# Performance work log

Hardware: AMD Instinct MI355X
Metric: run time of the kernel (lower is better)

Reference implementation:

```python
import jax, jax.numpy as jnp
import numpy as np

B, S, D = 2, 2048, 2048
H, KV = 16, 4          # n_heads, n_kv_heads
HD = D // H            # head_dim = 128
FFN = 5632
EPS = 1e-6


def rmsnorm(t, w):
    return (t * jax.lax.rsqrt(jnp.mean(t * t, axis=-1, keepdims=True) + EPS)) * w


def setup_inputs() -> dict:
    key = jax.random.key(0)
    ks = jax.random.split(key, 12)
    # rotary tables: cos/sin stacked in last dim -> [S, HD//2, 2]
    inv_freq = 1.0 / (10000.0 ** (np.arange(0, HD, 2, dtype=np.float32) / HD))
    t = np.arange(S, dtype=np.float32)
    ang = np.einsum('s,f->sf', t, inv_freq)
    freqs_cis = jnp.asarray(np.stack([np.cos(ang), np.sin(ang)], axis=-1))
    p = lambda k, shape: jax.random.normal(k, shape, dtype=jnp.float32) * 0.02
    return {
        'x': jax.random.normal(ks[0], (B, S, D), dtype=jnp.float32),
        'velocity': jnp.zeros((B, S, D), dtype=jnp.float32),
        'freqs_cis': freqs_cis,
        'pre_norm_w': jnp.ones((D,), jnp.float32),
        'wq': p(ks[1], (D, H * HD)),
        'wk': p(ks[2], (D, KV * HD)),
        'wv': p(ks[3], (D, KV * HD)),
        'wo': p(ks[4], (H * HD, D)),
        'q_norm_w': jnp.ones((HD,), jnp.float32),
        'k_norm_w': jnp.ones((HD,), jnp.float32),
        'log_beta': jnp.float32(np.log(0.5 / 0.5)),  # sigmoid -> 0.5
        'ffn_norm_w': jnp.ones((D,), jnp.float32),
        'w1': p(ks[5], (D, FFN)),
        'w3': p(ks[6], (D, FFN)),
        'w2': p(ks[7], (FFN, D)),
    }


def _rope(t, cos, sin):
    # t: [B,S,h,HD]; cos/sin broadcast [1,S,1,HD//2]
    tr = t.reshape(*t.shape[:-1], HD // 2, 2)
    t0, t1 = tr[..., 0], tr[..., 1]
    return jnp.stack([t0 * cos - t1 * sin, t0 * sin + t1 * cos], axis=-1).reshape(t.shape)


def reference(x, velocity, freqs_cis, pre_norm_w, wq, wk, wv, wo,
              q_norm_w, k_norm_w, log_beta, ffn_norm_w, w1, w3, w2):
    h = rmsnorm(x, pre_norm_w)
    q = (h @ wq).reshape(B, S, H, HD)
    k = (h @ wk).reshape(B, S, KV, HD)
    v = (h @ wv).reshape(B, S, KV, HD)
    # qk-norm (per-head RMSNorm), then rotary
    q = rmsnorm(q, q_norm_w)
    k = rmsnorm(k, k_norm_w)
    cos = freqs_cis[None, :, None, :, 0]
    sin = freqs_cis[None, :, None, :, 1]
    q = _rope(q, cos, sin)
    k = _rope(k, cos, sin)
    # GQA: repeat kv heads
    k = jnp.repeat(k, H // KV, axis=2)
    v = jnp.repeat(v, H // KV, axis=2)
    scores = jnp.einsum('bqhd,bkhd->bhqk', q, k) / jnp.float32(np.sqrt(HD))
    # exclusive self-attention: attend strictly to past (j < i); row 0 -> zeros
    excl = jnp.tril(jnp.ones((S, S), bool), k=-1)
    probs = jax.nn.softmax(jnp.where(excl, scores, jnp.float32(-1e30)), axis=-1)
    probs = probs * excl  # exact zeros on masked cols; row 0 fully zero
    attn_out = jnp.einsum('bhqk,bkhd->bqhd', probs, v).reshape(B, S, D) @ wo
    # sigmoid-gated momentum residual with clamp
    beta = jax.nn.sigmoid(log_beta)
    velocity = jnp.clip(beta * velocity + attn_out, -8.0, 8.0)
    x = x + velocity
    # inlined RMSNorm recompute + SwiGLU FFN
    normed = rmsnorm(x, ffn_norm_w)
    ffn = (jax.nn.silu(normed @ w1) * (normed @ w3)) @ w2
    return (x + ffn, velocity)
```

## Files before the change

kernel.cpp:

```cpp
#include <hip/hip_runtime.h>
#include <cstdint>
#include <cstddef>

typedef __bf16 bf16;
typedef __bf16 bf16x2 __attribute__((ext_vector_type(2)));
typedef __bf16 bf16x8 __attribute__((ext_vector_type(8)));
typedef float  f32x4  __attribute__((ext_vector_type(4)));

#define DEV __device__ __forceinline__

constexpr int Bc = 2, Sc = 2048, Dc = 2048, Hc = 16, KVc = 4, HDc = 128, FFNc = 5632;
constexpr int Rc = Bc * Sc;

DEV void async16(const bf16* g, bf16* l) {
  __builtin_amdgcn_global_load_lds((const __attribute__((address_space(1))) void*)g,
                                   (__attribute__((address_space(3))) void*)l, 16, 0, 0);
}

__global__ void transpose_cast(const float* __restrict__ in, bf16* __restrict__ out,
                               int K, int N, int rowoff, int ldout) {
  __shared__ float tile[32][33];
  int k0 = blockIdx.y * 32, n0 = blockIdx.x * 32;
  int tx = threadIdx.x, ty = threadIdx.y;
  for (int r = ty; r < 32; r += 8)
    tile[r][tx] = in[(size_t)(k0 + r) * N + n0 + tx];
  __syncthreads();
  for (int r = ty; r < 32; r += 8)
    out[(size_t)(rowoff + n0 + r) * ldout + k0 + tx] = (bf16)tile[tx][r];
}

__global__ void transpose_v(const bf16* __restrict__ qkvb, bf16* __restrict__ vht) {
  __shared__ bf16 tile[32][33];
  int s0 = blockIdx.x * 32, d0 = blockIdx.y * 32, bg = blockIdx.z;
  int tx = threadIdx.x, ty = threadIdx.y;
  int b = bg >> 2, g = bg & 3;
  const bf16* src = qkvb + (size_t)(b * Sc) * 3072 + 2560 + g * 128;
  for (int r = ty; r < 32; r += 8)
    tile[r][tx] = src[(size_t)(s0 + r) * 3072 + d0 + tx];
  __syncthreads();
  bf16* dst = vht + ((size_t)bg * HDc) * Sc;
  for (int r = ty; r < 32; r += 8)
    dst[(size_t)(d0 + r) * Sc + s0 + tx] = tile[tx][r];
}

__global__ void rmsnorm_cast(const float* __restrict__ x, const float* __restrict__ w,
                             bf16* __restrict__ out) {
  __shared__ float red[4];
  int row = blockIdx.x, tid = threadIdx.x;
  const float* xr = x + (size_t)row * Dc;
  float ss = 0.f;
#pragma unroll
  for (int i = 0; i < Dc / 256; ++i) { float v = xr[tid + i * 256]; ss += v * v; }
  for (int off = 32; off; off >>= 1) ss += __shfl_xor(ss, off);
  if ((tid & 63) == 0) red[tid >> 6] = ss;
  __syncthreads();
  float rstd = rsqrtf((red[0] + red[1] + red[2] + red[3]) * (1.f / Dc) + 1e-6f);
  bf16* orow = out + (size_t)row * Dc;
#pragma unroll
  for (int i = 0; i < Dc / 256; ++i) {
    int j = tid + i * 256;
    orow[j] = (bf16)(xr[j] * rstd * w[j]);
  }
}

DEV int swzofs(int r, int quad) {
  int pr = r >> 1;
  int g = (((r & 1) << 2) | quad) ^ (pr & 7);
  return pr * 64 + g * 8;
}

template <int MODE, int NF>
__global__ __launch_bounds__(512, 2) void gemm256(
    const bf16* __restrict__ A, int lda, const bf16* __restrict__ Bt,
    float* __restrict__ Cf, bf16* __restrict__ Cb,
    const float* __restrict__ xin, const float* __restrict__ velin,
    const float* __restrict__ lbp, float* __restrict__ velout,
    int K, int ldc, int nbx) {
  constexpr int BN = NF * 64;
  constexpr int BLD = 2 + BN / 128;
  __shared__ bf16 Asb[3][256 * 32];
  __shared__ bf16 Bsb[3][BN * 32];
  const int tid = threadIdx.x, lane = tid & 63, w = tid >> 6;
  const int quad = lane >> 4, l15 = lane & 15;
  const int wm = w >> 2, wn = w & 3;

  const int nwg = gridDim.x, bid = blockIdx.x;
  const int qq = nwg >> 3, rr = nwg & 7, xcd = bid & 7, lid = bid >> 3;
  const int swz = (xcd < rr ? xcd * (qq + 1) : rr * (qq + 1) + (xcd - rr) * qq) + lid;
  const int m0 = (swz / nbx) * 256, n0 = (swz % nbx) * BN;

  const int NT = K >> 5;

  f32x4 acc[8][NF];
  const f32x4 zf = {0.f, 0.f, 0.f, 0.f};
#pragma unroll
  for (int i = 0; i < 8; ++i)
#pragma unroll
    for (int j = 0; j < NF; ++j) acc[i][j] = zf;

  auto stage = [&](int kt, int ring) {
    const int k0 = kt * 32;
#pragma unroll
    for (int i = 0; i < 2; ++i) {
      int fi = w * 2 + i;
      int pr = fi * 8 + (lane >> 3), g0 = (lane & 7) ^ (pr & 7);
      int r = pr * 2 + (g0 >> 2), c8 = (g0 & 3) * 8;
      async16(A + (size_t)(m0 + r) * lda + k0 + c8, Asb[ring] + fi * 512);
    }
#pragma unroll
    for (int i = 0; i < BN / 128; ++i) {
      int fi = w * (BN / 128) + i;
      int pr = fi * 8 + (lane >> 3), g0 = (lane & 7) ^ (pr & 7);
      int r = pr * 2 + (g0 >> 2), c8 = (g0 & 3) * 8;
      async16(Bt + (size_t)(n0 + r) * K + k0 + c8, Bsb[ring] + fi * 512);
    }
  };

  stage(0, 0);
  stage(1, 1);
  if constexpr (BLD == 4) asm volatile("s_waitcnt vmcnt(4)" ::: "memory");
  else                    asm volatile("s_waitcnt vmcnt(3)" ::: "memory");
  __builtin_amdgcn_s_barrier();

  int r0 = 0;
  for (int kt = 0; kt < NT; ++kt) {
    int r2 = r0 + 2; if (r2 >= 3) r2 -= 3;
    const bf16* Ak = Asb[r0];
    const bf16* Bk = Bsb[r0];
    if (kt + 2 < NT) stage(kt + 2, r2);

    bf16x8 bfr[NF], af[4];
#pragma unroll
    for (int j = 0; j < NF; ++j)
      bfr[j] = *(const bf16x8*)(Bk + swzofs(wn * (NF * 16) + j * 16 + l15, quad));
#pragma unroll
    for (int i = 0; i < 4; ++i)
      af[i] = *(const bf16x8*)(Ak + swzofs(wm * 128 + i * 16 + l15, quad));
    __builtin_amdgcn_s_barrier();
    __builtin_amdgcn_s_setprio(1);
#pragma unroll
    for (int i = 0; i < 4; ++i)
#pragma unroll
      for (int j = 0; j < NF; ++j)
        acc[i][j] = __builtin_amdgcn_mfma_f32_16x16x32_bf16(af[i], bfr[j], acc[i][j], 0, 0, 0);
    __builtin_amdgcn_s_setprio(0);
    __builtin_amdgcn_s_barrier();

#pragma unroll
    for (int i = 0; i < 4; ++i)
      af[i] = *(const bf16x8*)(Ak + swzofs(wm * 128 + 64 + i * 16 + l15, quad));
    __builtin_amdgcn_s_barrier();
    __builtin_amdgcn_s_setprio(1);
#pragma unroll
    for (int i = 0; i < 4; ++i)
#pragma unroll
      for (int j = 0; j < NF; ++j)
        acc[4 + i][j] = __builtin_amdgcn_mfma_f32_16x16x32_bf16(af[i], bfr[j], acc[4 + i][j], 0, 0, 0);
    __builtin_amdgcn_s_setprio(0);

    if (kt + 2 < NT) {
      if constexpr (BLD == 4) asm volatile("s_waitcnt vmcnt(4)" ::: "memory");
      else                    asm volatile("s_waitcnt vmcnt(3)" ::: "memory");
    } else if (kt + 2 == NT) {
      asm volatile("s_waitcnt vmcnt(0)" ::: "memory");
    }
    __builtin_amdgcn_sched_barrier(0);
    __builtin_amdgcn_s_barrier();
    r0 = (r0 == 2) ? 0 : r0 + 1;
  }

  float beta = 0.f;
  if (MODE == 1) beta = 1.f / (1.f + __expf(-lbp[0]));
#pragma unroll
  for (int i = 0; i < 8; ++i) {
#pragma unroll
    for (int j = 0; j < NF; ++j) {
#pragma unroll
      for (int r = 0; r < 4; ++r) {
        int row = m0 + wm * 128 + i * 16 + quad * 4 + r;
        int col = n0 + wn * (NF * 16) + j * 16 + l15;
        size_t idx = (size_t)row * ldc + col;
        float c = acc[i][j][r];
        if (MODE == 1) {
          float v = beta * velin[idx] + c;
          v = fminf(8.f, fmaxf(-8.f, v));
          velout[idx] = v;
          Cf[idx] = xin[idx] + v;
        } else if (MODE == 2) {
          Cb[idx] = (bf16)c;
        } else {
          Cf[idx] = xin[idx] + c;
        }
      }
    }
  }
}

__global__ __launch_bounds__(256) void qk_norm_rope(
    const bf16* __restrict__ qkv, const float* __restrict__ qw, const float* __restrict__ kw,
    const float* __restrict__ freqs, bf16* __restrict__ qh, bf16* __restrict__ kh) {
  int row = blockIdx.x;
  int b = row >> 11, s = row & 2047;
  int tid = threadIdx.x, wvid = tid >> 6, lane = tid & 63;
  float cs = freqs[(size_t)(s * 64 + lane) * 2 + 0];
  float sn = freqs[(size_t)(s * 64 + lane) * 2 + 1];
  for (int slot = wvid; slot < 20; slot += 4) {
    const bf16* base = qkv + (size_t)row * 3072 + slot * 128;
    float t0 = (float)base[2 * lane], t1 = (float)base[2 * lane + 1];
    float ss = t0 * t0 + t1 * t1;
    for (int off = 32; off; off >>= 1) ss += __shfl_xor(ss, off);
    float rstd = rsqrtf(ss * (1.f / 128.f) + 1e-6f);
    const float* w = (slot < 16) ? qw : kw;
    float sc = (slot < 16) ? 0.08838834764831845f : 1.f;
    float n0 = t0 * rstd * w[2 * lane], n1 = t1 * rstd * w[2 * lane + 1];
    bf16x2 o;
    o[0] = (bf16)((n0 * cs - n1 * sn) * sc);
    o[1] = (bf16)((n0 * sn + n1 * cs) * sc);
    if (slot < 16)
      *(bf16x2*)(qh + ((size_t)(b * Hc + slot) * Sc + s) * HDc + 2 * lane) = o;
    else
      *(bf16x2*)(kh + ((size_t)(b * KVc + (slot - 16)) * Sc + s) * HDc + 2 * lane) = o;
  }
}

__global__ __launch_bounds__(256) void flash_attn(
    const bf16* __restrict__ qh, const bf16* __restrict__ kh, const bf16* __restrict__ vht,
    bf16* __restrict__ attn) {
  __shared__ bf16 Ks[2][64 * 128];
  __shared__ bf16 Vs[2][128 * 64];
  __shared__ bf16 Ps[4][16 * 68];
  const int tid = threadIdx.x, lane = tid & 63, wvid = tid >> 6;
  const int quad = lane >> 4, l15 = lane & 15;
  const int pairp = blockIdx.x;
  const int h = blockIdx.y, b = blockIdx.z, g = h >> 2;
  const bf16* qbase = qh + (size_t)(b * Hc + h) * Sc * HDc;
  const bf16* kbase = kh + (size_t)(b * KVc + g) * Sc * HDc;
  const bf16* vbase = vht + (size_t)(b * KVc + g) * HDc * Sc;
  const f32x4 zf = {0.f, 0.f, 0.f, 0.f};
  bf16* pw = Ps[wvid];

  bf16x8 ones;
#pragma unroll
  for (int e = 0; e < 8; ++e) ones[e] = (bf16)1.0f;

  int kcol[4], vcol[2];
#pragma unroll
  for (int f = 0; f < 4; ++f) kcol[f] = ((f * 64 + quad * 16) ^ (l15 << 4)) >> 1;
#pragma unroll
  for (int ks = 0; ks < 2; ++ks) vcol[ks] = ((ks * 64 + quad * 16) ^ ((l15 & 7) << 4)) >> 1;

  auto stage = [&](int kt2, int bsel) {
    const int k0s = kt2 * 64;
#pragma unroll
    for (int r = 0; r < 4; ++r) {
      int krow = (wvid * 4 + r) * 4 + quad;
      const bf16* src = kbase + (size_t)(k0s + krow) * HDc + ((l15 ^ (krow & 15)) * 8);
      async16(src, &Ks[bsel][(wvid * 4 + r) * 512]);
    }
#pragma unroll
    for (int r = 0; r < 4; ++r) {
      int vrow = (wvid * 4 + r) * 8 + (lane >> 3);
      int c8 = lane & 7;
      const bf16* src = vbase + (size_t)vrow * Sc + k0s + ((c8 ^ (vrow & 7)) * 8);
      async16(src, &Vs[bsel][(wvid * 4 + r) * 512]);
    }
  };

  for (int pass = 0; pass < 2; ++pass) {
    const int qt = pass ? 31 - pairp : pairp;
    const int q0 = qt * 64 + wvid * 16;

    bf16x8 qf[4];
#pragma unroll
    for (int f = 0; f < 4; ++f)
      qf[f] = *(const bf16x8*)(qbase + (size_t)(q0 + l15) * HDc + f * 32 + quad * 8);

    f32x4 Oa[8];
#pragma unroll
    for (int i = 0; i < 8; ++i) Oa[i] = zf;
    float m_i[4], l_i[4];
#pragma unroll
    for (int r = 0; r < 4; ++r) { m_i[r] = -3e38f; l_i[r] = 0.f; }

    const int ntiles = qt + 1;

    __syncthreads();
    stage(0, 0);

    for (int kt = 0; kt < ntiles; ++kt) {
      const int buf = kt & 1;
      const int k0 = kt * 64;
      __syncthreads();
      if (kt + 1 < ntiles) stage(kt + 1, buf ^ 1);

      f32x4 sc[4];
#pragma unroll
      for (int ks = 0; ks < 4; ++ks) {
        sc[ks] = zf;
#pragma unroll
        for (int f = 0; f < 4; ++f) {
          bf16x8 kf = *(const bf16x8*)(&Ks[buf][ks * 2048 + l15 * 128 + kcol[f]]);
          sc[ks] = __builtin_amdgcn_mfma_f32_16x16x32_bf16(qf[f], kf, sc[ks], 0, 0, 0);
        }
      }

      if (kt == qt) {
#pragma unroll
        for (int r = 0; r < 4; ++r) {
          int qg = q0 + quad * 4 + r;
#pragma unroll
          for (int ks = 0; ks < 4; ++ks)
            if (k0 + ks * 16 + l15 >= qg) sc[ks][r] = -3e38f;
        }
      }

      float mx[4], al[4];
#pragma unroll
      for (int r = 0; r < 4; ++r)
        mx[r] = fmaxf(fmaxf(sc[0][r], sc[1][r]), fmaxf(sc[2][r], sc[3][r]));
#pragma unroll
      for (int off = 8; off; off >>= 1)
#pragma unroll
        for (int r = 0; r < 4; ++r) mx[r] = fmaxf(mx[r], __shfl_xor(mx[r], off));
#pragma unroll
      for (int r = 0; r < 4; ++r) {
        float mn = fmaxf(m_i[r], mx[r]);
        al[r] = __expf(m_i[r] - mn);
        m_i[r] = mn;
#pragma unroll
        for (int ks = 0; ks < 4; ++ks) {
          float p = (sc[ks][r] > -1e37f) ? __expf(sc[ks][r] - mn) : 0.f;
          sc[ks][r] = p;
        }
      }

#pragma unroll
      for (int r = 0; r < 4; ++r)
#pragma unroll
        for (int ks = 0; ks < 4; ++ks)
          pw[(quad * 4 + r) * 68 + ks * 16 + l15] = (bf16)sc[ks][r];

#pragma unroll
      for (int i = 0; i < 8; ++i)
#pragma unroll
        for (int r = 0; r < 4; ++r) Oa[i][r] *= al[r];

      bf16x8 pf0 = *(const bf16x8*)(pw + l15 * 68 + quad * 8);
      bf16x8 pf1 = *(const bf16x8*)(pw + l15 * 68 + 32 + quad * 8);

      f32x4 ls = zf;
      ls = __builtin_amdgcn_mfma_f32_16x16x32_bf16(pf0, ones, ls, 0, 0, 0);
      ls = __builtin_amdgcn_mfma_f32_16x16x32_bf16(pf1, ones, ls, 0, 0, 0);

#pragma unroll
      for (int i = 0; i < 8; ++i) {
        bf16x8 vf0 = *(const bf16x8*)(&Vs[buf][(i * 16 + l15) * 64 + vcol[0]]);
        Oa[i] = __builtin_amdgcn_mfma_f32_16x16x32_bf16(pf0, vf0, Oa[i], 0, 0, 0);
        bf16x8 vf1 = *(const bf16x8*)(&Vs[buf][(i * 16 + l15) * 64 + vcol[1]]);
        Oa[i] = __builtin_amdgcn_mfma_f32_16x16x32_bf16(pf1, vf1, Oa[i], 0, 0, 0);
      }
#pragma unroll
      for (int r = 0; r < 4; ++r) l_i[r] = l_i[r] * al[r] + ls[r];
    }

#pragma unroll
    for (int r = 0; r < 4; ++r) {
      float inv = (l_i[r] > 0.f) ? 1.f / l_i[r] : 0.f;
      int qg = q0 + quad * 4 + r;
      bf16* orow = attn + (size_t)(b * Sc + qg) * Dc + h * HDc;
#pragma unroll
      for (int i = 0; i < 8; ++i) orow[i * 16 + l15] = (bf16)(Oa[i][r] * inv);
    }
  }
}

__global__ __launch_bounds__(256) void silu_mul_ip(bf16* __restrict__ g) {
  int row = blockIdx.y * 4 + (threadIdx.x >> 6);
  int j0 = (blockIdx.x * 64 + (threadIdx.x & 63)) * 8;
  bf16* p = g + (size_t)row * (2 * FFNc) + j0;
  const bf16x8 a = *(const bf16x8*)p;
  const bf16x8 bb = *(const bf16x8*)(p + FFNc);
  bf16x8 o;
#pragma unroll
  for (int e = 0; e < 8; ++e) {
    float xa = (float)a[e], xb = (float)bb[e];
    float s = xa / (1.f + __expf(-xa));
    o[e] = (bf16)(s * xb);
  }
  *(bf16x8*)p = o;
}

extern "C" void kernel_launch(void* const* d_in, const int* in_sizes, int n_in,
                              void* d_out, int out_size, void* d_ws, size_t ws_size,
                              hipStream_t stream) {
  (void)in_sizes; (void)n_in; (void)out_size; (void)ws_size;
  const float* x    = (const float*)d_in[0];
  const float* vel  = (const float*)d_in[1];
  const float* frq  = (const float*)d_in[2];
  const float* prew = (const float*)d_in[3];
  const float* wq   = (const float*)d_in[4];
  const float* wk   = (const float*)d_in[5];
  const float* wvw  = (const float*)d_in[6];
  const float* wo   = (const float*)d_in[7];
  const float* qnw  = (const float*)d_in[8];
  const float* knw  = (const float*)d_in[9];
  const float* lb   = (const float*)d_in[10];
  const float* ffnw = (const float*)d_in[11];
  const float* w1   = (const float*)d_in[12];
  const float* w3   = (const float*)d_in[13];
  const float* w2   = (const float*)d_in[14];

  float* out0 = (float*)d_out;
  float* out1 = out0 + (size_t)Rc * Dc;

  char* ws = (char*)d_ws;
  bf16* W  = (bf16*)ws;
  bf16* R1 = (bf16*)(ws + (size_t)23068672);
  bf16* G  = (bf16*)(ws + (size_t)23068672 + 16777216);
  bf16* hbuf   = R1;
  bf16* attn   = R1;
  bf16* normed = R1;
  bf16* qkvb   = G;
  bf16* qhb    = G + (size_t)4096 * 3072;
  bf16* khb    = qhb + (size_t)2 * 16 * 2048 * 128;
  bf16* vht    = khb + (size_t)2 * 4 * 2048 * 128;
  bf16* gbuf   = G;

  dim3 tb(32, 8);

  transpose_cast<<<dim3(64, 64), tb, 0, stream>>>(wq, W, 2048, 2048, 0, 2048);
  transpose_cast<<<dim3(16, 64), tb, 0, stream>>>(wk, W, 2048, 512, 2048, 2048);
  transpose_cast<<<dim3(16, 64), tb, 0, stream>>>(wvw, W, 2048, 512, 2560, 2048);
  rmsnorm_cast<<<Rc, 256, 0, stream>>>(x, prew, hbuf);
  gemm256<2, 4><<<192, 512, 0, stream>>>(hbuf, 2048, W, nullptr, qkvb, nullptr, nullptr,
                                         nullptr, nullptr, 2048, 3072, 12);
  qk_norm_rope<<<Rc, 256, 0, stream>>>(qkvb, qnw, knw, frq, qhb, khb);
  transpose_v<<<dim3(64, 4, 8), tb, 0, stream>>>(qkvb, vht);

  flash_attn<<<dim3(16, Hc, Bc), 256, 0, stream>>>(qhb, khb, vht, attn);
  transpose_cast<<<dim3(64, 64), tb, 0, stream>>>(wo, W, 2048, 2048, 0, 2048);
  gemm256<1, 2><<<256, 512, 0, stream>>>(attn, 2048, W, out0, nullptr, x, vel, lb, out1,
                                         2048, 2048, 16);

  rmsnorm_cast<<<Rc, 256, 0, stream>>>(out0, ffnw, normed);
  transpose_cast<<<dim3(176, 64), tb, 0, stream>>>(w1, W, 2048, 5632, 0, 2048);
  gemm256<2, 2><<<704, 512, 0, stream>>>(normed, 2048, W, nullptr, gbuf, nullptr, nullptr,
                                         nullptr, nullptr, 2048, 11264, 44);
  transpose_cast<<<dim3(176, 64), tb, 0, stream>>>(w3, W, 2048, 5632, 0, 2048);
  gemm256<2, 2><<<704, 512, 0, stream>>>(normed, 2048, W, nullptr, gbuf + FFNc, nullptr,
                                         nullptr, nullptr, nullptr, 2048, 11264, 44);
  silu_mul_ip<<<dim3(11, 1024), 256, 0, stream>>>(gbuf);
  transpose_cast<<<dim3(64, 176), tb, 0, stream>>>(w2, W, 5632, 2048, 0, 5632);
  gemm256<3, 2><<<256, 512, 0, stream>>>(gbuf, 11264, W, out0, nullptr, out0, nullptr,
                                         nullptr, nullptr, 5632, 2048, 16);
}
```

Baseline: 1.052 ms.

## Rework GEMM to 64-wide K tiles with a new swizzle and restructured pipeline

Replaces the templated 256xBN GEMM with a fixed 256x128 tile GEMM that stages 64-wide K slices per iteration, halving the loop trip count and the number of barriers per unit of work. It precomputes per-thread source pointers with an XOR row swizzle, and moves the wait and barrier to the top of each iteration. It also issues the next prefetch after the fragment loads. The QKV projection now uses 128-wide N tiles with twice as many blocks, which improves CU coverage. The cost is a larger LDS footprint (3-stage ring of 64-wide slices) and more live fragment registers, which may affect occupancy.

```diff
diff --git a/kernel.cpp b/kernel.cpp
--- a/kernel.cpp
+++ b/kernel.cpp
@@ -63,23 +63,15 @@
   }
 }
 
-DEV int swzofs(int r, int quad) {
-  int pr = r >> 1;
-  int g = (((r & 1) << 2) | quad) ^ (pr & 7);
-  return pr * 64 + g * 8;
-}
-
-template <int MODE, int NF>
-__global__ __launch_bounds__(512, 2) void gemm256(
+template <int MODE>
+__global__ __launch_bounds__(512, 2) void gemm128(
     const bf16* __restrict__ A, int lda, const bf16* __restrict__ Bt,
     float* __restrict__ Cf, bf16* __restrict__ Cb,
     const float* __restrict__ xin, const float* __restrict__ velin,
     const float* __restrict__ lbp, float* __restrict__ velout,
     int K, int ldc, int nbx) {
-  constexpr int BN = NF * 64;
-  constexpr int BLD = 2 + BN / 128;
-  __shared__ bf16 Asb[3][256 * 32];
-  __shared__ bf16 Bsb[3][BN * 32];
+  __shared__ bf16 Asb[3][2 * 8192];
+  __shared__ bf16 Bsb[3][8192];
   const int tid = threadIdx.x, lane = tid & 63, w = tid >> 6;
   const int quad = lane >> 4, l15 = lane & 15;
   const int wm = w >> 2, wn = w & 3;
@@ -87,85 +79,104 @@
   const int nwg = gridDim.x, bid = blockIdx.x;
   const int qq = nwg >> 3, rr = nwg & 7, xcd = bid & 7, lid = bid >> 3;
   const int swz = (xcd < rr ? xcd * (qq + 1) : rr * (qq + 1) + (xcd - rr) * qq) + lid;
-  const int m0 = (swz / nbx) * 256, n0 = (swz % nbx) * BN;
-
-  const int NT = K >> 5;
-
-  f32x4 acc[8][NF];
+  const int m0 = (swz / nbx) * 256, n0 = (swz % nbx) * 128;
+
+  const int NT = K >> 6;
+
+  f32x4 acc[8][2];
   const f32x4 zf = {0.f, 0.f, 0.f, 0.f};
 #pragma unroll
-  for (int i = 0; i < 8; ++i)
-#pragma unroll
-    for (int j = 0; j < NF; ++j) acc[i][j] = zf;
-
-  auto stage = [&](int kt, int ring) {
-    const int k0 = kt * 32;
-#pragma unroll
-    for (int i = 0; i < 2; ++i) {
-      int fi = w * 2 + i;
-      int pr = fi * 8 + (lane >> 3), g0 = (lane & 7) ^ (pr & 7);
-      int r = pr * 2 + (g0 >> 2), c8 = (g0 & 3) * 8;
-      async16(A + (size_t)(m0 + r) * lda + k0 + c8, Asb[ring] + fi * 512);
-    }
-#pragma unroll
-    for (int i = 0; i < BN / 128; ++i) {
-      int fi = w * (BN / 128) + i;
-      int pr = fi * 8 + (lane >> 3), g0 = (lane & 7) ^ (pr & 7);
-      int r = pr * 2 + (g0 >> 2), c8 = (g0 & 3) * 8;
-      async16(Bt + (size_t)(n0 + r) * K + k0 + c8, Bsb[ring] + fi * 512);
-    }
+  for (int i = 0; i < 8; ++i) { acc[i][0] = zf; acc[i][1] = zf; }
+
+  const int srow = tid >> 3, schk = tid & 7;
+  const bf16* srcA[2][2];
+  const bf16* srcB[2];
+#pragma unroll
+  for (int h = 0; h < 2; ++h)
+#pragma unroll
+    for (int j = 0; j < 2; ++j) {
+      int row = h * 128 + j * 64 + srow;
+      srcA[h][j] = A + (size_t)(m0 + row) * lda + ((schk ^ (row & 7)) * 8);
+    }
+#pragma unroll
+  for (int j = 0; j < 2; ++j) {
+    int row = j * 64 + srow;
+    srcB[j] = Bt + (size_t)(n0 + row) * K + ((schk ^ (row & 7)) * 8);
+  }
+
+  auto stage = [&](int t, int ring) {
+    const int koff = t * 64;
+    bf16* Al = Asb[ring];
+    bf16* Bl = Bsb[ring];
+#pragma unroll
+    for (int h = 0; h < 2; ++h)
+#pragma unroll
+      for (int j = 0; j < 2; ++j)
+        async16(srcA[h][j] + koff, Al + h * 8192 + j * 4096 + w * 512);
+#pragma unroll
+    for (int j = 0; j < 2; ++j)
+      async16(srcB[j] + koff, Bl + j * 4096 + w * 512);
   };
+
+  const int ac0 = ((quad) ^ (l15 & 7)) * 8;
+  const int ac1 = ((4 + quad) ^ (l15 & 7)) * 8;
 
   stage(0, 0);
   stage(1, 1);
-  if constexpr (BLD == 4) asm volatile("s_waitcnt vmcnt(4)" ::: "memory");
-  else                    asm volatile("s_waitcnt vmcnt(3)" ::: "memory");
-  __builtin_amdgcn_s_barrier();
 
   int r0 = 0;
-  for (int kt = 0; kt < NT; ++kt) {
-    int r2 = r0 + 2; if (r2 >= 3) r2 -= 3;
-    const bf16* Ak = Asb[r0];
-    const bf16* Bk = Bsb[r0];
-    if (kt + 2 < NT) stage(kt + 2, r2);
-
-    bf16x8 bfr[NF], af[4];
-#pragma unroll
-    for (int j = 0; j < NF; ++j)
-      bfr[j] = *(const bf16x8*)(Bk + swzofs(wn * (NF * 16) + j * 16 + l15, quad));
-#pragma unroll
-    for (int i = 0; i < 4; ++i)
-      af[i] = *(const bf16x8*)(Ak + swzofs(wm * 128 + i * 16 + l15, quad));
+  for (int t = 0; t < NT; ++t) {
+    if (t == NT - 1) asm volatile("s_waitcnt vmcnt(0)" ::: "memory");
+    else             asm volatile("s_waitcnt vmcnt(6)" ::: "memory");
+    __builtin_amdgcn_s_barrier();
+
+    const bf16* Ab = Asb[r0] + wm * 8192;
+    const bf16* Bb = Bsb[r0];
+
+    bf16x8 af[4][2], bfr[2][2];
+#pragma unroll
+    for (int i = 0; i < 4; ++i) {
+      af[i][0] = *(const bf16x8*)(Ab + (i * 16 + l15) * 64 + ac0);
+      af[i][1] = *(const bf16x8*)(Ab + (i * 16 + l15) * 64 + ac1);
+    }
+#pragma unroll
+    for (int nf = 0; nf < 2; ++nf) {
+      bfr[nf][0] = *(const bf16x8*)(Bb + (wn * 32 + nf * 16 + l15) * 64 + ac0);
+      bfr[nf][1] = *(const bf16x8*)(Bb + (wn * 32 + nf * 16 + l15) * 64 + ac1);
+    }
+    {
+      int r2 = r0 + 2; if (r2 >= 3) r2 -= 3;
+      if (t + 2 < NT) stage(t + 2, r2);
+    }
+    __builtin_amdgcn_sched_barrier(0);
     __builtin_amdgcn_s_barrier();
     __builtin_amdgcn_s_setprio(1);
 #pragma unroll
-    for (int i = 0; i < 4; ++i)
-#pragma unroll
-      for (int j = 0; j < NF; ++j)
-        acc[i][j] = __builtin_amdgcn_mfma_f32_16x16x32_bf16(af[i], bfr[j], acc[i][j], 0, 0, 0);
+    for (int kh = 0; kh < 2; ++kh)
+#pragma unroll
+      for (int i = 0; i < 4; ++i)
+#pragma unroll
+        for (int nf = 0; nf < 2; ++nf)
+          acc[i][nf] = __builtin_amdgcn_mfma_f32_16x16x32_bf16(af[i][kh], bfr[nf][kh], acc[i][nf], 0, 0, 0);
     __builtin_amdgcn_s_setprio(0);
-    __builtin_amdgcn_s_barrier();
-
-#pragma unroll
-    for (int i = 0; i < 4; ++i)
-      af[i] = *(const bf16x8*)(Ak + swzofs(wm * 128 + 64 + i * 16 + l15, quad));
+
+#pragma unroll
+    for (int i = 0; i < 4; ++i) {
+      af[i][0] = *(const bf16x8*)(Ab + ((i + 4) * 16 + l15) * 64 + ac0);
+      af[i][1] = *(const bf16x8*)(Ab + ((i + 4) * 16 + l15) * 64 + ac1);
+    }
+    __builtin_amdgcn_sched_barrier(0);
     __builtin_amdgcn_s_barrier();
     __builtin_amdgcn_s_setprio(1);
 #pragma unroll
-    for (int i = 0; i < 4; ++i)
-#pragma unroll
-      for (int j = 0; j < NF; ++j)
-        acc[4 + i][j] = __builtin_amdgcn_mfma_f32_16x16x32_bf16(af[i], bfr[j], acc[4 + i][j], 0, 0, 0);
+    for (int kh = 0; kh < 2; ++kh)
+#pragma unroll
+      for (int i = 0; i < 4; ++i)
+#pragma unroll
+        for (int nf = 0; nf < 2; ++nf)
+          acc[4 + i][nf] = __builtin_amdgcn_mfma_f32_16x16x32_bf16(af[i][kh], bfr[nf][kh], acc[4 + i][nf], 0, 0, 0);
     __builtin_amdgcn_s_setprio(0);
 
-    if (kt + 2 < NT) {
-      if constexpr (BLD == 4) asm volatile("s_waitcnt vmcnt(4)" ::: "memory");
-      else                    asm volatile("s_waitcnt vmcnt(3)" ::: "memory");
-    } else if (kt + 2 == NT) {
-      asm volatile("s_waitcnt vmcnt(0)" ::: "memory");
-    }
-    __builtin_amdgcn_sched_barrier(0);
-    __builtin_amdgcn_s_barrier();
     r0 = (r0 == 2) ? 0 : r0 + 1;
   }
 
@@ -174,13 +185,13 @@
 #pragma unroll
   for (int i = 0; i < 8; ++i) {
 #pragma unroll
-    for (int j = 0; j < NF; ++j) {
+    for (int nf = 0; nf < 2; ++nf) {
 #pragma unroll
       for (int r = 0; r < 4; ++r) {
         int row = m0 + wm * 128 + i * 16 + quad * 4 + r;
-        int col = n0 + wn * (NF * 16) + j * 16 + l15;
+        int col = n0 + wn * 32 + nf * 16 + l15;
         size_t idx = (size_t)row * ldc + col;
-        float c = acc[i][j][r];
+        float c = acc[i][nf][r];
         if (MODE == 1) {
           float v = beta * velin[idx] + c;
           v = fminf(8.f, fmaxf(-8.f, v));
@@ -432,25 +443,25 @@
   transpose_cast<<<dim3(16, 64), tb, 0, stream>>>(wk, W, 2048, 512, 2048, 2048);
   transpose_cast<<<dim3(16, 64), tb, 0, stream>>>(wvw, W, 2048, 512, 2560, 2048);
   rmsnorm_cast<<<Rc, 256, 0, stream>>>(x, prew, hbuf);
-  gemm256<2, 4><<<192, 512, 0, stream>>>(hbuf, 2048, W, nullptr, qkvb, nullptr, nullptr,
-                                         nullptr, nullptr, 2048, 3072, 12);
+  gemm128<2><<<384, 512, 0, stream>>>(hbuf, 2048, W, nullptr, qkvb, nullptr, nullptr,
+                                      nullptr, nullptr, 2048, 3072, 24);
   qk_norm_rope<<<Rc, 256, 0, stream>>>(qkvb, qnw, knw, frq, qhb, khb);
   transpose_v<<<dim3(64, 4, 8), tb, 0, stream>>>(qkvb, vht);
 
   flash_attn<<<dim3(16, Hc, Bc), 256, 0, stream>>>(qhb, khb, vht, attn);
   transpose_cast<<<dim3(64, 64), tb, 0, stream>>>(wo, W, 2048, 2048, 0, 2048);
-  gemm256<1, 2><<<256, 512, 0, stream>>>(attn, 2048, W, out0, nullptr, x, vel, lb, out1,
-                                         2048, 2048, 16);
+  gemm128<1><<<256, 512, 0, stream>>>(attn, 2048, W, out0, nullptr, x, vel, lb, out1,
+                                      2048, 2048, 16);
 
   rmsnorm_cast<<<Rc, 256, 0, stream>>>(out0, ffnw, normed);
   transpose_cast<<<dim3(176, 64), tb, 0, stream>>>(w1, W, 2048, 5632, 0, 2048);
-  gemm256<2, 2><<<704, 512, 0, stream>>>(normed, 2048, W, nullptr, gbuf, nullptr, nullptr,
-                                         nullptr, nullptr, 2048, 11264, 44);
+  gemm128<2><<<704, 512, 0, stream>>>(normed, 2048, W, nullptr, gbuf, nullptr, nullptr,
+                                      nullptr, nullptr, 2048, 11264, 44);
   transpose_cast<<<dim3(176, 64), tb, 0, stream>>>(w3, W, 2048, 5632, 0, 2048);
-  gemm256<2, 2><<<704, 512, 0, stream>>>(normed, 2048, W, nullptr, gbuf + FFNc, nullptr,
-                                         nullptr, nullptr, nullptr, 2048, 11264, 44);
+  gemm128<2><<<704, 512, 0, stream>>>(normed, 2048, W, nullptr, gbuf + FFNc, nullptr,
+                                      nullptr, nullptr, nullptr, 2048, 11264, 44);
   silu_mul_ip<<<dim3(11, 1024), 256, 0, stream>>>(gbuf);
   transpose_cast<<<dim3(64, 176), tb, 0, stream>>>(w2, W, 5632, 2048, 0, 5632);
-  gemm256<3, 2><<<256, 512, 0, stream>>>(gbuf, 11264, W, out0, nullptr, out0, nullptr,
-                                         nullptr, nullptr, 5632, 2048, 16);
-}
+  gemm128<3><<<256, 512, 0, stream>>>(gbuf, 11264, W, out0, nullptr, out0, nullptr,
+                                      nullptr, nullptr, 5632, 2048, 16);
+}
```

Measured after the change: 936.0 us. -11.0%, faster.
